# Performance work log

Hardware: AMD Instinct MI355X
Metric: run time of the kernel (lower is better)

Reference implementation:

```python
import jax, jax.numpy as jnp
import numpy as np

N_NODES = 100000
N_EDGES = 1600000
N_GRAPHS = 64
INS = 2
HID = 64


def setup_inputs() -> dict:
    key = jax.random.key(0)
    ks = jax.random.split(key, 16)
    def lin(k, fin, fout):
        # torch Linear default init: U(-1/sqrt(fin), 1/sqrt(fin)); stored as (in, out)
        bound = 1.0 / np.sqrt(fin)
        k1, k2 = jax.random.split(k)
        W = jax.random.uniform(k1, (fin, fout), jnp.float32, -bound, bound)
        b = jax.random.uniform(k2, (fout,), jnp.float32, -bound, bound)
        return W, b
    W1, b1 = lin(ks[0], INS + 1, HID)
    W2, b2 = lin(ks[1], HID, HID)
    W3, b3 = lin(ks[2], HID, HID)
    W4, b4 = lin(ks[3], HID + 3, HID + 3)
    W5, b5 = lin(ks[4], HID + 3, INS)
    x = jax.random.normal(ks[5], (N_NODES, INS), jnp.float32)
    edge_index = jax.random.randint(ks[6], (2, N_EDGES), 0, N_NODES, jnp.int64)
    edge_attr = jax.random.normal(ks[7], (N_EDGES, 1), jnp.float32)
    u = jax.random.normal(ks[8], (N_GRAPHS,), jnp.float32)
    batch = jnp.sort(jax.random.randint(ks[9], (N_NODES,), 0, N_GRAPHS, jnp.int64))
    return {"x": x, "edge_index": edge_index, "edge_attr": edge_attr, "u": u,
            "batch": batch, "W1": W1, "b1": b1, "W2": W2, "b2": b2,
            "W3": W3, "b3": b3, "W4": W4, "b4": b4, "W5": W5, "b5": b5}


def reference(x, edge_index, edge_attr, u, batch, W1, b1, W2, b2, W3, b3, W4, b4, W5, b5):
    src, dest = edge_index[0], edge_index[1]
    n = x.shape[0]
    # edge MLP on gathered source features + edge attr  [E, ins+1] -> [E, HID]
    h = jnp.concatenate([x[src], edge_attr], axis=1)
    h = jax.nn.relu(h @ W1 + b1)
    h = jax.nn.relu(h @ W2 + b2)
    h = h @ W3 + b3
    # scatter_mean over destination nodes (torch_scatter semantics: empty -> 0)
    summed = jax.ops.segment_sum(h, dest, num_segments=n)
    cnt = jax.ops.segment_sum(jnp.ones((h.shape[0],), h.dtype), dest, num_segments=n)
    agg = summed / jnp.maximum(cnt, 1.0)[:, None]
    # node MLP with global feature broadcast  [N, ins+HID+1] -> [N, ins]
    z = jnp.concatenate([x, agg, u[batch][:, None]], axis=1)
    z = jax.nn.relu(z @ W4 + b4)
    return z @ W5 + b5
```

## Files before the change

### kernel.cpp

```cpp
#include <hip/hip_runtime.h>

constexpr int HID = 64;
constexpr int BN_SHIFT = 6;
constexpr int BROWS = 1 << BN_SHIFT;
constexpr int CAP = 2048;
constexpr int CH = 4096;
constexpr int NBMAX = 2048;
constexpr float FPSCALE = 262144.f;
constexpr float INV_FPSCALE = 1.f / 262144.f;

typedef __attribute__((ext_vector_type(8))) short s8v;
typedef __attribute__((ext_vector_type(4))) float f32x4;
typedef __attribute__((ext_vector_type(4))) unsigned int u32x4;

__device__ __forceinline__ s8v as_s8(u32x4 v) { s8v r; __builtin_memcpy(&r, &v, 16); return r; }

__global__ __launch_bounds__(64) void pack_kernel(
    const float* __restrict__ W2,
    const float* __restrict__ W3, const float* __restrict__ b3,
    const float* __restrict__ W4, const float* __restrict__ b4,
    unsigned short* __restrict__ Bhi, unsigned short* __restrict__ Blo,
    unsigned short* __restrict__ Cbhi, unsigned short* __restrict__ Cblo,
    float* __restrict__ b4p, int* __restrict__ bcur, int NB)
{
    const int blk = blockIdx.x;
    const int k = threadIdx.x;
    const int gid = blk * 64 + k;
    if (gid < NB) bcur[gid] = gid * CAP;
    if (blk < 64) {
        const float w = W2[k * 64 + blk];
        const unsigned int u = __float_as_uint(w);
        const float hf = __uint_as_float(u & 0xffff0000u);
        Bhi[blk * 64 + k] = (unsigned short)(u >> 16);
        Blo[blk * 64 + k] = (unsigned short)(__float_as_uint(w - hf) >> 16);
    } else {
        const int j = blk - 64;
        float s = 0.f;
        if (j < 67)
            for (int m = 0; m < 64; ++m)
                s = fmaf(W3[k * 64 + m], W4[(2 + m) * 67 + j], s);
        const unsigned int usv = __float_as_uint(s);
        const float hf = __uint_as_float(usv & 0xffff0000u);
        Cbhi[j * 64 + k] = (unsigned short)(usv >> 16);
        Cblo[j * 64 + k] = (unsigned short)(__float_as_uint(s - hf) >> 16);
        if (k == 0) {
            float t = 0.f;
            if (j < 67) {
                t = b4[j];
                for (int m = 0; m < 64; ++m) t = fmaf(b3[m], W4[(2 + m) * 67 + j], t);
            }
            b4p[j] = t;
        }
    }
}

__global__ __launch_bounds__(256) void binA_kernel(
    const int* __restrict__ ei, const float* __restrict__ x,
    const float* __restrict__ ea, int* __restrict__ bcur,
    float4* __restrict__ A, int E, int NB)
{
    __shared__ int hist[NBMAX];
    __shared__ int base_s[NBMAX];
    const int tid = threadIdx.x;
    const int e0 = blockIdx.x * CH;

    int dcache[CH / 256];
    for (int i = tid; i < NB; i += 256) hist[i] = 0;
    __syncthreads();
    #pragma unroll
    for (int r = 0; r < CH / 256; ++r) {
        const int e = e0 + r * 256 + tid;
        dcache[r] = (e < E) ? ei[E + e] : -1;
        if (dcache[r] >= 0) atomicAdd(&hist[dcache[r] >> BN_SHIFT], 1);
    }
    __syncthreads();
    for (int i = tid; i < NB; i += 256) {
        const int h = hist[i];
        base_s[i] = h ? atomicAdd(&bcur[i], h) : 0;
        hist[i] = 0;
    }
    __syncthreads();
    #pragma unroll
    for (int r = 0; r < CH / 256; ++r) {
        const int e = e0 + r * 256 + tid;
        const int d = dcache[r];
        if (d >= 0) {
            const int src = ei[e];
            const float w = ea[e];
            const float2 xv = ((const float2*)x)[src];
            const int b = d >> BN_SHIFT;
            const int pos = base_s[b] + atomicAdd(&hist[b], 1);
            if (pos < (b + 1) * CAP)
                A[pos] = make_float4(xv.x, xv.y, w, __int_as_float(d));
        }
    }
}

__global__ __launch_bounds__(256, 2) void bucket_kernel(
    const float4* __restrict__ A, const int* __restrict__ bcur,
    const float* __restrict__ W1, const float* __restrict__ b1,
    const unsigned short* __restrict__ Bhi, const unsigned short* __restrict__ Blo,
    const float* __restrict__ b2,
    const float* __restrict__ x, const float* __restrict__ u,
    const int* __restrict__ batch,
    const float* __restrict__ W4, const float* __restrict__ W5,
    const float* __restrict__ b5,
    const unsigned short* __restrict__ Cbhi, const unsigned short* __restrict__ Cblo,
    const float* __restrict__ b4p,
    float* __restrict__ out, int N)
{
    __shared__ int aggl[BROWS * 65];
    __shared__ __align__(16) unsigned int stg[4 * 2048];
    __shared__ float wsm[6 * 80];
    const int b = blockIdx.x;
    const int lo = b << BN_SHIFT;
    const int span = min(BROWS, N - lo);
    const int start = b * CAP;
    const int end = min(bcur[b], start + CAP);
    const int tid = threadIdx.x;

    for (int i = tid; i < BROWS * 65; i += 256) aggl[i] = 0;
    for (int i = tid; i < 480; i += 256) {
        const int grp = i / 80, c = i % 80;
        float v = 0.f;
        if (c < 67) {
            if      (grp == 0) v = W4[c];
            else if (grp == 1) v = W4[67 + c];
            else if (grp == 2) v = W4[66 * 67 + c];
            else if (grp == 3) v = W5[2 * c];
            else if (grp == 4) v = W5[2 * c + 1];
            else               v = b4p[c];
        }
        wsm[i] = v;
    }
    __syncthreads();

    const int wv = tid >> 6, lane = tid & 63;
    const int am = lane & 15, aq = lane >> 4;
    const int rsw = (lane & 7) << 4;
    unsigned int* stw = stg + wv * 2048;
    char* stb = (char*)stw;

    float bias[4];
    #pragma unroll
    for (int fb = 0; fb < 4; ++fb) bias[fb] = b2[fb * 16 + am];

    const float4 ginval = make_float4(0.f, 0.f, 0.f, __int_as_float(-1));
    int i = start + (wv << 6) + lane;
    float4 g = ginval;
    if (i < end) g = A[i];

    const int nIter = (end - start + 255) >> 8;
    for (int it = 0; it < nIter; ++it) {
        const int inext = i + 256;
        float4 gn = ginval;
        if (inext < end) gn = A[inext];

        const float gx0 = g.x, gx1 = g.y, gea = g.z;
        const int dstl = __float_as_int(g.w) - lo;
        if (dstl >= 0) atomicAdd(&aggl[dstl * 65 + 64], 1);

        f32x4 acc[4][4];
        #pragma unroll
        for (int a = 0; a < 4; ++a)
            #pragma unroll
            for (int c = 0; c < 4; ++c) acc[a][c] = (f32x4){0.f, 0.f, 0.f, 0.f};

        #pragma unroll
        for (int kb = 0; kb < 2; ++kb) {
            #pragma unroll
            for (int jc = 0; jc < 4; ++jc) {
                unsigned int hp[4], lp[4];
                #pragma unroll
                for (int jp = 0; jp < 4; ++jp) {
                    const int j0 = kb * 32 + jc * 8 + jp * 2;
                    float v0 = fmaf(gx0, W1[j0],     fmaf(gx1, W1[64 + j0],     fmaf(gea, W1[128 + j0],     b1[j0])));
                    float v1 = fmaf(gx0, W1[j0 + 1], fmaf(gx1, W1[64 + j0 + 1], fmaf(gea, W1[128 + j0 + 1], b1[j0 + 1])));
                    v0 = fmaxf(v0, 0.f); v1 = fmaxf(v1, 0.f);
                    const unsigned int u0 = __float_as_uint(v0), u1 = __float_as_uint(v1);
                    hp[jp] = (u0 >> 16) | (u1 & 0xffff0000u);
                    const float r0 = v0 - __uint_as_float(u0 & 0xffff0000u);
                    const float r1 = v1 - __uint_as_float(u1 & 0xffff0000u);
                    lp[jp] = (__float_as_uint(r0) >> 16) | (__float_as_uint(r1) & 0xffff0000u);
                }
                const int boffb = (lane * 128 + jc * 16) ^ rsw;
                *(uint4*)(stb + boffb)        = make_uint4(hp[0], hp[1], hp[2], hp[3]);
                *(uint4*)(stb + (boffb ^ 64)) = make_uint4(lp[0], lp[1], lp[2], lp[3]);
            }

            s8v ah[4], al[4], bh[4], bl[4];
            #pragma unroll
            for (int eb = 0; eb < 4; ++eb) {
                const int ar = eb * 16 + am;
                const int ao = (ar * 128 + aq * 16) ^ ((ar & 7) << 4);
                ah[eb] = *(const s8v*)(stb + ao);
                al[eb] = *(const s8v*)(stb + (ao ^ 64));
            }
            #pragma unroll
            for (int fb = 0; fb < 4; ++fb) {
                const int bo = (fb * 16 + am) * 64 + kb * 32 + aq * 8;
                bh[fb] = *(const s8v*)(Bhi + bo);
                bl[fb] = *(const s8v*)(Blo + bo);
            }
            asm volatile("" ::: "memory");

            #pragma unroll
            for (int eb = 0; eb < 4; ++eb)
                #pragma unroll
                for (int fb = 0; fb < 4; ++fb) {
                    acc[eb][fb] = __builtin_amdgcn_mfma_f32_16x16x32_bf16(ah[eb], bh[fb], acc[eb][fb], 0, 0, 0);
                    acc[eb][fb] = __builtin_amdgcn_mfma_f32_16x16x32_bf16(ah[eb], bl[fb], acc[eb][fb], 0, 0, 0);
                    acc[eb][fb] = __builtin_amdgcn_mfma_f32_16x16x32_bf16(al[eb], bh[fb], acc[eb][fb], 0, 0, 0);
                }
        }
        asm volatile("" ::: "memory");

        #pragma unroll
        for (int eb = 0; eb < 4; ++eb) {
            #pragma unroll
            for (int r = 0; r < 4; ++r) {
                const int drow = __shfl(dstl, eb * 16 + aq * 4 + r);
                if (drow >= 0) {
                    #pragma unroll
                    for (int fb = 0; fb < 4; ++fb) {
                        const float v = fmaxf(acc[eb][fb][r] + bias[fb], 0.f);
                        atomicAdd(&aggl[drow * 65 + fb * 16 + am], __float2int_rn(v * FPSCALE));
                    }
                }
            }
        }
        g = gn;
        i = inext;
    }
    __syncthreads();

    {
        const int myrow = wv * 16 + am;
        const float cnt = (float)aggl[myrow * 65 + 64];
        const float inv = INV_FPSCALE / fmaxf(cnt, 1.f);

        s8v mh[2], ml[2];
        #pragma unroll
        for (int kb = 0; kb < 2; ++kb) {
            unsigned int hp[4], lp[4];
            #pragma unroll
            for (int jp = 0; jp < 4; ++jp) {
                const int k0 = kb * 32 + aq * 8 + jp * 2;
                const float v0 = (float)aggl[myrow * 65 + k0] * inv;
                const float v1 = (float)aggl[myrow * 65 + k0 + 1] * inv;
                const unsigned int u0 = __float_as_uint(v0), u1 = __float_as_uint(v1);
                hp[jp] = (u0 >> 16) | (u1 & 0xffff0000u);
                const float r0 = v0 - __uint_as_float(u0 & 0xffff0000u);
                const float r1 = v1 - __uint_as_float(u1 & 0xffff0000u);
                lp[jp] = (__float_as_uint(r0) >> 16) | (__float_as_uint(r1) & 0xffff0000u);
            }
            mh[kb] = as_s8((u32x4){hp[0], hp[1], hp[2], hp[3]});
            ml[kb] = as_s8((u32x4){lp[0], lp[1], lp[2], lp[3]});
        }

        float2 xs[4]; float us[4];
        #pragma unroll
        for (int r = 0; r < 4; ++r) {
            int nd = lo + wv * 16 + aq * 4 + r;
            if (nd >= N) nd = N - 1;
            xs[r] = ((const float2*)x)[nd];
            us[r] = u[batch[nd]];
        }

        float o0[4] = {0.f, 0.f, 0.f, 0.f}, o1[4] = {0.f, 0.f, 0.f, 0.f};
        #pragma unroll
        for (int ct = 0; ct < 5; ++ct) {
            f32x4 d = (f32x4){0.f, 0.f, 0.f, 0.f};
            #pragma unroll
            for (int kb = 0; kb < 2; ++kb) {
                const int co = (ct * 16 + am) * 64 + kb * 32 + aq * 8;
                const s8v cbh = *(const s8v*)(Cbhi + co);
                const s8v cbl = *(const s8v*)(Cblo + co);
                d = __builtin_amdgcn_mfma_f32_16x16x32_bf16(mh[kb], cbh, d, 0, 0, 0);
                d = __builtin_amdgcn_mfma_f32_16x16x32_bf16(mh[kb], cbl, d, 0, 0, 0);
                d = __builtin_amdgcn_mfma_f32_16x16x32_bf16(ml[kb], cbh, d, 0, 0, 0);
            }
            const int col = ct * 16 + am;
            const float w40 = wsm[col], w41 = wsm[80 + col], w4u = wsm[160 + col];
            const float w5a = wsm[240 + col], w5b = wsm[320 + col], bb = wsm[400 + col];
            #pragma unroll
            for (int r = 0; r < 4; ++r) {
                float z = d[r] + bb;
                z = fmaf(xs[r].x, w40, z);
                z = fmaf(xs[r].y, w41, z);
                z = fmaf(us[r], w4u, z);
                z = fmaxf(z, 0.f);
                o0[r] = fmaf(z, w5a, o0[r]);
                o1[r] = fmaf(z, w5b, o1[r]);
            }
        }
        #pragma unroll
        for (int r = 0; r < 4; ++r) {
            #pragma unroll
            for (int m = 1; m < 16; m <<= 1) {
                o0[r] += __shfl_xor(o0[r], m);
                o1[r] += __shfl_xor(o1[r], m);
            }
        }
        if (am == 0) {
            #pragma unroll
            for (int r = 0; r < 4; ++r) {
                const int rr = wv * 16 + aq * 4 + r;
                if (rr < span) {
                    out[2 * (lo + rr)]     = o0[r] + b5[0];
                    out[2 * (lo + rr) + 1] = o1[r] + b5[1];
                }
            }
        }
    }
}

extern "C" void kernel_launch(void* const* d_in, const int* in_sizes, int n_in,
                              void* d_out, int out_size, void* d_ws, size_t ws_size,
                              hipStream_t stream) {
    const float* x     = (const float*)d_in[0];
    const int*   ei    = (const int*)  d_in[1];
    const float* ea    = (const float*)d_in[2];
    const float* u     = (const float*)d_in[3];
    const int*   batch = (const int*)  d_in[4];
    const float* W1 = (const float*)d_in[5];  const float* b1 = (const float*)d_in[6];
    const float* W2 = (const float*)d_in[7];  const float* b2 = (const float*)d_in[8];
    const float* W3 = (const float*)d_in[9];  const float* b3 = (const float*)d_in[10];
    const float* W4 = (const float*)d_in[11]; const float* b4 = (const float*)d_in[12];
    const float* W5 = (const float*)d_in[13]; const float* b5 = (const float*)d_in[14];

    const int N = in_sizes[0] / 2;
    const int E = in_sizes[2];
    const int NB = (N + BROWS - 1) >> BN_SHIFT;

    char* w = (char*)d_ws;
    size_t o = 0;
    int* bcur = (int*)(w + o); o += NBMAX * 4;
    o = (o + 15) & ~(size_t)15;
    unsigned short* Bhi  = (unsigned short*)(w + o); o += 64 * 64 * 2;
    unsigned short* Blo  = (unsigned short*)(w + o); o += 64 * 64 * 2;
    unsigned short* Cbhi = (unsigned short*)(w + o); o += 80 * 64 * 2;
    unsigned short* Cblo = (unsigned short*)(w + o); o += 80 * 64 * 2;
    float* b4p = (float*)(w + o); o += 80 * 4;
    o = (o + 15) & ~(size_t)15;
    float4* Abuf = (float4*)(w + o); o += (size_t)NB * CAP * 16;

    const int nCH = (E + CH - 1) / CH;

    pack_kernel<<<144, 64, 0, stream>>>(W2, W3, b3, W4, b4, Bhi, Blo, Cbhi, Cblo, b4p, bcur, NB);
    binA_kernel<<<nCH, 256, 0, stream>>>(ei, x, ea, bcur, Abuf, E, NB);
    bucket_kernel<<<NB, 256, 0, stream>>>(Abuf, bcur, W1, b1, Bhi, Blo, b2,
                                          x, u, batch, W4, W5, b5,
                                          Cbhi, Cblo, b4p,
                                          (float*)d_out, N);
}
```

Baseline: 154.9 us.

## Build MFMA A-operand fragments in registers via shuffles instead of LDS staging

Each lane now computes the first-layer activations directly in the MFMA A-fragment layout. It takes its edge's features from other lanes with shuffles and keeps W1/b1 slices in registers. This drops the per-wave LDS staging buffer along with its write/read round trip and the hoisted global weight loads inside the loop. The cost is more register pressure, three shuffles per edge block, and B-operand loads moved into the inner loop. Lower LDS use may also allow higher occupancy.

```diff
diff --git a/kernel.cpp b/kernel.cpp
--- a/kernel.cpp
+++ b/kernel.cpp
@@ -110,7 +110,6 @@
     float* __restrict__ out, int N)
 {
     __shared__ int aggl[BROWS * 65];
-    __shared__ __align__(16) unsigned int stg[4 * 2048];
     __shared__ float wsm[6 * 80];
     const int b = blockIdx.x;
     const int lo = b << BN_SHIFT;
@@ -137,9 +136,20 @@
 
     const int wv = tid >> 6, lane = tid & 63;
     const int am = lane & 15, aq = lane >> 4;
-    const int rsw = (lane & 7) << 4;
-    unsigned int* stw = stg + wv * 2048;
-    char* stb = (char*)stw;
+
+    float w1x[2][8], w1y[2][8], w1z[2][8], w1b[2][8];
+    #pragma unroll
+    for (int kb = 0; kb < 2; ++kb) {
+        const int j0 = kb * 32 + aq * 8;
+        *(float4*)&w1x[kb][0] = *(const float4*)(W1 + j0);
+        *(float4*)&w1x[kb][4] = *(const float4*)(W1 + j0 + 4);
+        *(float4*)&w1y[kb][0] = *(const float4*)(W1 + 64 + j0);
+        *(float4*)&w1y[kb][4] = *(const float4*)(W1 + 64 + j0 + 4);
+        *(float4*)&w1z[kb][0] = *(const float4*)(W1 + 128 + j0);
+        *(float4*)&w1z[kb][4] = *(const float4*)(W1 + 128 + j0 + 4);
+        *(float4*)&w1b[kb][0] = *(const float4*)(b1 + j0);
+        *(float4*)&w1b[kb][4] = *(const float4*)(b1 + j0 + 4);
+    }
 
     float bias[4];
     #pragma unroll
@@ -160,6 +170,14 @@
         const int dstl = __float_as_int(g.w) - lo;
         if (dstl >= 0) atomicAdd(&aggl[dstl * 65 + 64], 1);
 
+        float gex[4], gey[4], gez[4];
+        #pragma unroll
+        for (int eb = 0; eb < 4; ++eb) {
+            gex[eb] = __shfl(gx0, eb * 16 + am);
+            gey[eb] = __shfl(gx1, eb * 16 + am);
+            gez[eb] = __shfl(gea, eb * 16 + am);
+        }
+
         f32x4 acc[4][4];
         #pragma unroll
         for (int a = 0; a < 4; ++a)
@@ -169,13 +187,16 @@
         #pragma unroll
         for (int kb = 0; kb < 2; ++kb) {
             #pragma unroll
-            for (int jc = 0; jc < 4; ++jc) {
+            for (int eb = 0; eb < 4; ++eb) {
                 unsigned int hp[4], lp[4];
                 #pragma unroll
                 for (int jp = 0; jp < 4; ++jp) {
-                    const int j0 = kb * 32 + jc * 8 + jp * 2;
-                    float v0 = fmaf(gx0, W1[j0],     fmaf(gx1, W1[64 + j0],     fmaf(gea, W1[128 + j0],     b1[j0])));
-                    float v1 = fmaf(gx0, W1[j0 + 1], fmaf(gx1, W1[64 + j0 + 1], fmaf(gea, W1[128 + j0 + 1], b1[j0 + 1])));
+                    float v0 = fmaf(gex[eb], w1x[kb][2*jp],
+                               fmaf(gey[eb], w1y[kb][2*jp],
+                               fmaf(gez[eb], w1z[kb][2*jp], w1b[kb][2*jp])));
+                    float v1 = fmaf(gex[eb], w1x[kb][2*jp+1],
+                               fmaf(gey[eb], w1y[kb][2*jp+1],
+                               fmaf(gez[eb], w1z[kb][2*jp+1], w1b[kb][2*jp+1])));
                     v0 = fmaxf(v0, 0.f); v1 = fmaxf(v1, 0.f);
                     const unsigned int u0 = __float_as_uint(v0), u1 = __float_as_uint(v1);
                     hp[jp] = (u0 >> 16) | (u1 & 0xffff0000u);
@@ -183,37 +204,19 @@
                     const float r1 = v1 - __uint_as_float(u1 & 0xffff0000u);
                     lp[jp] = (__float_as_uint(r0) >> 16) | (__float_as_uint(r1) & 0xffff0000u);
                 }
-                const int boffb = (lane * 128 + jc * 16) ^ rsw;
-                *(uint4*)(stb + boffb)        = make_uint4(hp[0], hp[1], hp[2], hp[3]);
-                *(uint4*)(stb + (boffb ^ 64)) = make_uint4(lp[0], lp[1], lp[2], lp[3]);
-            }
-
-            s8v ah[4], al[4], bh[4], bl[4];
-            #pragma unroll
-            for (int eb = 0; eb < 4; ++eb) {
-                const int ar = eb * 16 + am;
-                const int ao = (ar * 128 + aq * 16) ^ ((ar & 7) << 4);
-                ah[eb] = *(const s8v*)(stb + ao);
-                al[eb] = *(const s8v*)(stb + (ao ^ 64));
-            }
-            #pragma unroll
-            for (int fb = 0; fb < 4; ++fb) {
-                const int bo = (fb * 16 + am) * 64 + kb * 32 + aq * 8;
-                bh[fb] = *(const s8v*)(Bhi + bo);
-                bl[fb] = *(const s8v*)(Blo + bo);
-            }
-            asm volatile("" ::: "memory");
-
-            #pragma unroll
-            for (int eb = 0; eb < 4; ++eb)
+                const s8v ah = as_s8((u32x4){hp[0], hp[1], hp[2], hp[3]});
+                const s8v al = as_s8((u32x4){lp[0], lp[1], lp[2], lp[3]});
                 #pragma unroll
                 for (int fb = 0; fb < 4; ++fb) {
-                    acc[eb][fb] = __builtin_amdgcn_mfma_f32_16x16x32_bf16(ah[eb], bh[fb], acc[eb][fb], 0, 0, 0);
-                    acc[eb][fb] = __builtin_amdgcn_mfma_f32_16x16x32_bf16(ah[eb], bl[fb], acc[eb][fb], 0, 0, 0);
-                    acc[eb][fb] = __builtin_amdgcn_mfma_f32_16x16x32_bf16(al[eb], bh[fb], acc[eb][fb], 0, 0, 0);
+                    const int bo = (fb * 16 + am) * 64 + kb * 32 + aq * 8;
+                    const s8v bh = *(const s8v*)(Bhi + bo);
+                    const s8v bl = *(const s8v*)(Blo + bo);
+                    acc[eb][fb] = __builtin_amdgcn_mfma_f32_16x16x32_bf16(ah, bh, acc[eb][fb], 0, 0, 0);
+                    acc[eb][fb] = __builtin_amdgcn_mfma_f32_16x16x32_bf16(ah, bl, acc[eb][fb], 0, 0, 0);
+                    acc[eb][fb] = __builtin_amdgcn_mfma_f32_16x16x32_bf16(al, bh, acc[eb][fb], 0, 0, 0);
                 }
-        }
-        asm volatile("" ::: "memory");
+            }
+        }
 
         #pragma unroll
         for (int eb = 0; eb < 4; ++eb) {
```

Measured after the change: 143.4 us. -7.5%, faster.
